# Kernel tuning notes

Measured on AMD Instinct MI355X. Metric: run time of the kernel, lower is better.

The kernel has to match this reference:

```python
import jax, jax.numpy as jnp
import numpy as np

B, S, D, H = 2, 2048, 1024, 16
DK = D // H


def setup_inputs() -> dict:
    key = jax.random.key(0)
    ks = jax.random.split(key, 11)
    s = 1.0 / np.sqrt(D)
    inp = {
        "q": jax.random.normal(ks[0], (B, S, D), jnp.float32),
        "k": jax.random.normal(ks[1], (B, S, D), jnp.float32),
        "v": jax.random.normal(ks[2], (B, S, D), jnp.float32),
        # causal (lower-triangular) decoder mask, broadcast over batch & heads
        "mask": jnp.tril(jnp.ones((S, S), jnp.int32))[None, None, :, :],
        "Wq": jax.random.normal(ks[3], (D, D), jnp.float32) * s,
        "bq": jax.random.normal(ks[4], (D,), jnp.float32) * s,
        "Wk": jax.random.normal(ks[5], (D, D), jnp.float32) * s,
        "bk": jax.random.normal(ks[6], (D,), jnp.float32) * s,
        "Wv": jax.random.normal(ks[7], (D, D), jnp.float32) * s,
        "bv": jax.random.normal(ks[8], (D,), jnp.float32) * s,
        "Wo": jax.random.normal(ks[9], (D, D), jnp.float32) * s,
        "bo": jax.random.normal(ks[10], (D,), jnp.float32) * s,
    }
    return inp


def reference(q, k, v, mask, Wq, bq, Wk, bk, Wv, bv, Wo, bo):
    # projections (nn.Linear: x @ W.T + b)
    def proj(x, W, b):
        return (x @ W.T + b).reshape(B, S, H, DK).transpose(0, 2, 1, 3)  # [B,H,S,DK]

    Q = proj(q, Wq, bq)
    K = proj(k, Wk, bk)
    V = proj(v, Wv, bv)

    scores = jnp.einsum("bhsd,bhtd->bhst", Q, K) / jnp.sqrt(jnp.float32(DK))
    scores = jnp.where(mask == 0, jnp.float32(-1e9), scores)
    attn = jax.nn.softmax(scores, axis=-1)  # dropout=0.0 -> identity
    ctx = jnp.einsum("bhst,bhtd->bhsd", attn, V)
    ctx = ctx.transpose(0, 2, 1, 3).reshape(B, S, D)
    return ctx @ Wo.T + bo
```

## Files before the change

kernel.cpp:

```cpp
#include <hip/hip_runtime.h>

typedef __bf16 bf16;
typedef __bf16 bf16x8 __attribute__((ext_vector_type(8)));
typedef float floatx4 __attribute__((ext_vector_type(4)));

#define NB 2
#define NS 2048
#define ND 1024
#define NH 16
#define NDK 64
#define NM (NB * NS)

__device__ __forceinline__ void async_cp16(const void* g, void* l) {
  __builtin_amdgcn_global_load_lds(
      (const __attribute__((address_space(1))) void*)g,
      (__attribute__((address_space(3))) void*)l, 16, 0, 0);
}

__device__ __forceinline__ bf16x8 cvt8(const float* p) {
  float4 lo = *(const float4*)p, hi = *(const float4*)(p + 4);
  bf16x8 o;
  o[0] = (bf16)lo.x; o[1] = (bf16)lo.y; o[2] = (bf16)lo.z; o[3] = (bf16)lo.w;
  o[4] = (bf16)hi.x; o[5] = (bf16)hi.y; o[6] = (bf16)hi.z; o[7] = (bf16)hi.w;
  return o;
}

struct CvtArgs {
  const float* src[8];
  bf16* dst[8];
  int nblk[8];
  int nseg;
};

__global__ __launch_bounds__(256) void cvt_kernel(CvtArgs a) {
  int b = blockIdx.x, seg = 0;
  while (seg < a.nseg - 1 && b >= a.nblk[seg]) { b -= a.nblk[seg]; ++seg; }
  const size_t idx = ((size_t)b * 256 + threadIdx.x) * 8;
  *(bf16x8*)(a.dst[seg] + idx) = cvt8(a.src[seg] + idx);
}

template <int TM, typename TA, typename TC>
__global__ __launch_bounds__(256) void gemm_dma(
    const TA* __restrict__ A0, const TA* __restrict__ A1, const TA* __restrict__ A2,
    const bf16* __restrict__ W0, const bf16* __restrict__ W1, const bf16* __restrict__ W2,
    const float* __restrict__ bias0, const float* __restrict__ bias1, const float* __restrict__ bias2,
    TC* __restrict__ C0, TC* __restrict__ C1, TC* __restrict__ C2)
{
  const int z = blockIdx.z;
  const TA* A = (z == 0) ? A0 : (z == 1) ? A1 : A2;
  const bf16* W = (z == 0) ? W0 : (z == 1) ? W1 : W2;
  const float* bias = (z == 0) ? bias0 : (z == 1) ? bias1 : bias2;
  TC* C = (z == 0) ? C0 : (z == 1) ? C1 : C2;

  __shared__ bf16 At[TM * 32];
  __shared__ bf16 Bt[128 * 32];

  const int tid = threadIdx.x;
  const int wave = tid >> 6, lane = tid & 63;
  const int q4 = lane >> 4, l15 = lane & 15;
  const int m0 = blockIdx.y * TM, n0 = blockIdx.x * 128;
  constexpr int WM = TM / 2;
  constexpr int MI = WM / 16;
  const int wm = (wave >> 1) * WM, wn = (wave & 1) * 64;

  floatx4 acc[MI][4] = {};

  const bf16* Wg = W + (size_t)(n0 + (lane >> 2)) * ND + (lane & 3) * 8;
  const bf16* Ag = nullptr;
  const float* Af = nullptr;
  const int srow = tid >> 2, sk = (tid & 3) * 8;
  if constexpr (sizeof(TA) == 2)
    Ag = (const bf16*)A + (size_t)(m0 + (lane >> 2)) * ND + (lane & 3) * 8;
  else
    Af = (const float*)A + (size_t)(m0 + srow) * ND + sk;

  for (int k0 = 0; k0 < ND; k0 += 32) {
    bf16x8 a0, a1;
    if constexpr (sizeof(TA) == 4) {
      a0 = cvt8(Af + k0);
      if constexpr (TM == 128) a1 = cvt8(Af + (size_t)64 * ND + k0);
    }
    __syncthreads();
#pragma unroll
    for (int c2 = 0; c2 < 2; ++c2) {
      const int c = wave * 2 + c2;
      async_cp16(Wg + (size_t)c * 16 * ND + k0, &Bt[c * 16 * 32]);
    }
    if constexpr (sizeof(TA) == 2) {
#pragma unroll
      for (int c2 = 0; c2 < TM / 64; ++c2) {
        const int c = wave * (TM / 64) + c2;
        async_cp16(Ag + (size_t)c * 16 * ND + k0, &At[c * 16 * 32]);
      }
    } else {
      *(bf16x8*)&At[srow * 32 + sk] = a0;
      if constexpr (TM == 128) *(bf16x8*)&At[(srow + 64) * 32 + sk] = a1;
    }
    __syncthreads();

    bf16x8 af[MI], bfr[4];
#pragma unroll
    for (int i = 0; i < MI; ++i)
      af[i] = *(const bf16x8*)&At[(wm + i * 16 + l15) * 32 + q4 * 8];
#pragma unroll
    for (int j = 0; j < 4; ++j)
      bfr[j] = *(const bf16x8*)&Bt[(wn + j * 16 + l15) * 32 + q4 * 8];
#pragma unroll
    for (int i = 0; i < MI; ++i)
#pragma unroll
      for (int j = 0; j < 4; ++j)
        acc[i][j] = __builtin_amdgcn_mfma_f32_16x16x32_bf16(af[i], bfr[j], acc[i][j], 0, 0, 0);
  }

#pragma unroll
  for (int j = 0; j < 4; ++j) {
    const int col = n0 + wn + j * 16 + l15;
    const float bv = bias[col];
#pragma unroll
    for (int i = 0; i < MI; ++i) {
      const int rowb = m0 + wm + i * 16 + q4 * 4;
#pragma unroll
      for (int r = 0; r < 4; ++r)
        C[(size_t)(rowb + r) * ND + col] = (TC)(acc[i][j][r] + bv);
    }
  }
}

#define NEGBIG (-1e30f)
#define LDV 72

__global__ __launch_bounds__(256) void attn_kernel(
    const bf16* __restrict__ Q, const bf16* __restrict__ K,
    const bf16* __restrict__ V, bf16* __restrict__ O)
{
  __shared__ bf16 vt[2][64 * LDV];
  __shared__ bf16 pbuf[4][16 * LDV];

  const int bx = blockIdx.x;
  const int h = blockIdx.y, b = blockIdx.z;
  const int tid = threadIdx.x, wave = tid >> 6, lane = tid & 63;
  const int q4 = lane >> 4, l15 = lane & 15;
  const int sl = lane;
  const int dbase = wave * 8;

  const bf16* kp = K + ((size_t)(b * NS) + l15) * ND + h * NDK + q4 * 8;
  const bf16* vp = V + ((size_t)(b * NS) + sl) * ND + h * NDK + dbase;

  bf16x8 qf[2];
  floatx4 oacc[4];
  float psum[4];
  bf16x8 kA[8], vA[2], kB[8], vB[2];

  auto ldK = [&](int j, bf16x8 (&kk)[8]) {
    const bf16* p = kp + (size_t)j * (64 * ND);
#pragma unroll
    for (int nf = 0; nf < 4; ++nf)
#pragma unroll
      for (int t = 0; t < 2; ++t)
        kk[nf * 2 + t] = *(const bf16x8*)(p + (size_t)nf * 16 * ND + t * 32);
  };
  auto ldV = [&](int j, bf16x8 (&vv)[2]) {
    const bf16* p = vp + (size_t)j * (64 * ND);
    vv[0] = *(const bf16x8*)(p);
    vv[1] = *(const bf16x8*)(p + 32);
  };

  auto body = [&](int j, int iq, bf16x8 (&kc)[8], bf16x8 (&vc)[2],
                  bf16x8 (&kn)[8], bf16x8 (&vn)[2]) {
    const int cur = j & 1;
#pragma unroll
    for (int it = 0; it < 2; ++it)
#pragma unroll
      for (int e = 0; e < 8; ++e)
        vt[cur][(dbase + it * 32 + e) * LDV + sl] = vc[it][e];

    floatx4 sf[4];
#pragma unroll
    for (int nf = 0; nf < 4; ++nf) {
      floatx4 s = {0.f, 0.f, 0.f, 0.f};
      s = __builtin_amdgcn_mfma_f32_16x16x32_bf16(qf[0], kc[nf * 2 + 0], s, 0, 0, 0);
      s = __builtin_amdgcn_mfma_f32_16x16x32_bf16(qf[1], kc[nf * 2 + 1], s, 0, 0, 0);
      sf[nf] = s;
    }

    if (j < iq) { ldK(j + 1, kn); ldV(j + 1, vn); }

    __syncthreads();

    if (j == iq) {
#pragma unroll
      for (int nf = 0; nf < 4; ++nf) {
        const int kc2 = nf * 16 + l15;
#pragma unroll
        for (int r = 0; r < 4; ++r)
          if (kc2 > wave * 16 + q4 * 4 + r) sf[nf][r] = NEGBIG;
      }
    }

#pragma unroll
    for (int nf = 0; nf < 4; ++nf)
#pragma unroll
      for (int r = 0; r < 4; ++r) {
        const float pv = exp2f(sf[nf][r]);
        psum[r] += pv;
        pbuf[wave][(q4 * 4 + r) * LDV + nf * 16 + l15] = (bf16)pv;
      }
    __asm__ __volatile__("s_waitcnt lgkmcnt(0)" ::: "memory");

#pragma unroll
    for (int nf = 0; nf < 4; ++nf)
#pragma unroll
      for (int t = 0; t < 2; ++t) {
        bf16x8 pa = *(const bf16x8*)&pbuf[wave][l15 * LDV + t * 32 + q4 * 8];
        bf16x8 vb = *(const bf16x8*)&vt[cur][(nf * 16 + l15) * LDV + t * 32 + q4 * 8];
        oacc[nf] = __builtin_amdgcn_mfma_f32_16x16x32_bf16(pa, vb, oacc[nf], 0, 0, 0);
      }
  };

  for (int ph = 0; ph < 2; ++ph) {
    const int iq = ph ? (31 - bx) : bx;
    __syncthreads();

    const size_t qrow0 = (size_t)(b * NS + iq * 64 + wave * 16 + l15);
#pragma unroll
    for (int t = 0; t < 2; ++t) {
      bf16x8 tmp = *(const bf16x8*)(Q + qrow0 * ND + h * NDK + t * 32 + q4 * 8);
#pragma unroll
      for (int e = 0; e < 8; ++e) qf[t][e] = (bf16)((float)tmp[e] * 0.180336880f);
    }

#pragma unroll
    for (int nf = 0; nf < 4; ++nf) oacc[nf] = floatx4{0.f, 0.f, 0.f, 0.f};
#pragma unroll
    for (int r = 0; r < 4; ++r) psum[r] = 0.f;

    ldK(0, kA); ldV(0, vA);
    for (int j = 0; j <= iq; ++j) {
      if ((j & 1) == 0) body(j, iq, kA, vA, kB, vB);
      else              body(j, iq, kB, vB, kA, vA);
    }

#pragma unroll
    for (int r = 0; r < 4; ++r)
#pragma unroll
      for (int off = 1; off < 16; off <<= 1) psum[r] += __shfl_xor(psum[r], off, 16);

#pragma unroll
    for (int nf = 0; nf < 4; ++nf)
#pragma unroll
      for (int r = 0; r < 4; ++r) {
        const int qrow = iq * 64 + wave * 16 + q4 * 4 + r;
        O[(size_t)(b * NS + qrow) * ND + h * NDK + nf * 16 + l15] =
            (bf16)(oacc[nf][r] / psum[r]);
      }
  }
}

extern "C" void kernel_launch(void* const* d_in, const int* in_sizes, int n_in,
                              void* d_out, int out_size, void* d_ws, size_t ws_size,
                              hipStream_t stream) {
  const float* q  = (const float*)d_in[0];
  const float* k  = (const float*)d_in[1];
  const float* v  = (const float*)d_in[2];
  const float* Wq = (const float*)d_in[4];
  const float* bq = (const float*)d_in[5];
  const float* Wk = (const float*)d_in[6];
  const float* bk = (const float*)d_in[7];
  const float* Wv = (const float*)d_in[8];
  const float* bv = (const float*)d_in[9];
  const float* Wo = (const float*)d_in[10];
  const float* bo = (const float*)d_in[11];
  float* out = (float*)d_out;
  char* w = (char*)d_ws;

  const dim3 attn_grid(NS / 128, NH, NB);

  if (ws_size >= (size_t)56 << 20) {
    bf16* xq = (bf16*)(w);
    bf16* xk = (bf16*)(w + ((size_t)8 << 20));
    bf16* xv = (bf16*)(w + ((size_t)16 << 20));
    bf16* wq = (bf16*)(w + ((size_t)24 << 20));
    bf16* wk = (bf16*)(w + ((size_t)26 << 20));
    bf16* wv = (bf16*)(w + ((size_t)28 << 20));
    bf16* wo = (bf16*)(w + ((size_t)30 << 20));
    bf16* Qb = (bf16*)(w + ((size_t)32 << 20));
    bf16* Kb = (bf16*)(w + ((size_t)40 << 20));
    bf16* Vb = (bf16*)(w + ((size_t)48 << 20));
    bf16* Ob = xq;

    CvtArgs ca{};
    const int b4 = (int)((size_t)NM * ND / 2048);
    const int b1 = (int)((size_t)ND * ND / 2048);
    ca.src[0] = q;  ca.dst[0] = xq; ca.nblk[0] = b4;
    ca.src[1] = k;  ca.dst[1] = xk; ca.nblk[1] = b4;
    ca.src[2] = v;  ca.dst[2] = xv; ca.nblk[2] = b4;
    ca.src[3] = Wq; ca.dst[3] = wq; ca.nblk[3] = b1;
    ca.src[4] = Wk; ca.dst[4] = wk; ca.nblk[4] = b1;
    ca.src[5] = Wv; ca.dst[5] = wv; ca.nblk[5] = b1;
    ca.src[6] = Wo; ca.dst[6] = wo; ca.nblk[6] = b1;
    ca.nseg = 7;
    cvt_kernel<<<3 * b4 + 4 * b1, 256, 0, stream>>>(ca);

    gemm_dma<128, bf16, bf16><<<dim3(8, 32, 3), 256, 0, stream>>>(
        xq, xk, xv, wq, wk, wv, bq, bk, bv, Qb, Kb, Vb);
    attn_kernel<<<attn_grid, 256, 0, stream>>>(Qb, Kb, Vb, Ob);
    gemm_dma<64, bf16, float><<<dim3(8, 64, 1), 256, 0, stream>>>(
        Ob, Ob, Ob, wo, wo, wo, bo, bo, bo, out, out, out);
  } else if (ws_size >= (size_t)40 << 20) {
    bf16* wq = (bf16*)(w);
    bf16* wk = (bf16*)(w + ((size_t)2 << 20));
    bf16* wv = (bf16*)(w + ((size_t)4 << 20));
    bf16* wo = (bf16*)(w + ((size_t)6 << 20));
    bf16* Qb = (bf16*)(w + ((size_t)8 << 20));
    bf16* Kb = (bf16*)(w + ((size_t)16 << 20));
    bf16* Vb = (bf16*)(w + ((size_t)24 << 20));
    bf16* Ob = (bf16*)(w + ((size_t)32 << 20));

    CvtArgs ca{};
    const int b1 = (int)((size_t)ND * ND / 2048);
    ca.src[0] = Wq; ca.dst[0] = wq; ca.nblk[0] = b1;
    ca.src[1] = Wk; ca.dst[1] = wk; ca.nblk[1] = b1;
    ca.src[2] = Wv; ca.dst[2] = wv; ca.nblk[2] = b1;
    ca.src[3] = Wo; ca.dst[3] = wo; ca.nblk[3] = b1;
    ca.nseg = 4;
    cvt_kernel<<<4 * b1, 256, 0, stream>>>(ca);

    gemm_dma<128, float, bf16><<<dim3(8, 32, 3), 256, 0, stream>>>(
        q, k, v, wq, wk, wv, bq, bk, bv, Qb, Kb, Vb);
    attn_kernel<<<attn_grid, 256, 0, stream>>>(Qb, Kb, Vb, Ob);
    gemm_dma<64, bf16, float><<<dim3(8, 64, 1), 256, 0, stream>>>(
        Ob, Ob, Ob, wo, wo, wo, bo, bo, bo, out, out, out);
  }
}
```

Before: 270.5 us.

## Split causal attention KV range across two blocks and combine partial sums

Splits each query tile's key range into two halves handled by separate blocks, doubling the attention grid, then adds a combine kernel that sums the partial outputs and divides by the summed softmax denominators. This raises parallelism across the GPU's compute units for the attention stage. The cost is an extra kernel launch, extra global traffic for the partial outputs and row sums, and rounding the partial outputs to bf16 before they are combined. The method relies on the existing no-max exp2 softmax, so the two partial results can be added directly.

```diff
diff --git a/kernel.cpp b/kernel.cpp
--- a/kernel.cpp
+++ b/kernel.cpp
@@ -126,8 +126,172 @@
   }
 }
 
-#define NEGBIG (-1e30f)
 #define LDV 72
+
+__global__ __launch_bounds__(256) void attn_split(
+    const bf16* __restrict__ Q, const bf16* __restrict__ K,
+    const bf16* __restrict__ V, bf16* __restrict__ Oh0,
+    bf16* __restrict__ Oh1, float* __restrict__ Ps)
+{
+  __shared__ bf16 vt[2][64 * LDV];
+  __shared__ bf16 pbuf[4][16 * LDV];
+
+  const int bx = blockIdx.x;
+  const int h = blockIdx.y;
+  const int b = blockIdx.z & 1, half = blockIdx.z >> 1;
+  bf16* Oh = half ? Oh1 : Oh0;
+  const int tid = threadIdx.x, wave = tid >> 6, lane = tid & 63;
+  const int q4 = lane >> 4, l15 = lane & 15;
+  const int sl = lane;
+  const int dbase = wave * 8;
+
+  const bf16* kp = K + ((size_t)(b * NS) + l15) * ND + h * NDK + q4 * 8;
+  const bf16* vp = V + ((size_t)(b * NS) + sl) * ND + h * NDK + dbase;
+
+  bf16x8 qf[2];
+  floatx4 oacc[4];
+  float psum[4];
+  bf16x8 kA[8], vA[2], kB[8], vB[2];
+
+  auto ldK = [&](int j, bf16x8 (&kk)[8]) {
+    const bf16* p = kp + (size_t)j * (64 * ND);
+#pragma unroll
+    for (int nf = 0; nf < 4; ++nf)
+#pragma unroll
+      for (int t = 0; t < 2; ++t)
+        kk[nf * 2 + t] = *(const bf16x8*)(p + (size_t)nf * 16 * ND + t * 32);
+  };
+  auto ldV = [&](int j, bf16x8 (&vv)[2]) {
+    const bf16* p = vp + (size_t)j * (64 * ND);
+    vv[0] = *(const bf16x8*)(p);
+    vv[1] = *(const bf16x8*)(p + 32);
+  };
+
+  auto body = [&](int j, int iq, int je, bf16x8 (&kc)[8], bf16x8 (&vc)[2],
+                  bf16x8 (&kn)[8], bf16x8 (&vn)[2]) {
+    const int cur = j & 1;
+#pragma unroll
+    for (int it = 0; it < 2; ++it)
+#pragma unroll
+      for (int e = 0; e < 8; ++e)
+        vt[cur][(dbase + it * 32 + e) * LDV + sl] = vc[it][e];
+
+    floatx4 sf[4];
+#pragma unroll
+    for (int nf = 0; nf < 4; ++nf) {
+      floatx4 s = {0.f, 0.f, 0.f, 0.f};
+      s = __builtin_amdgcn_mfma_f32_16x16x32_bf16(qf[0], kc[nf * 2 + 0], s, 0, 0, 0);
+      s = __builtin_amdgcn_mfma_f32_16x16x32_bf16(qf[1], kc[nf * 2 + 1], s, 0, 0, 0);
+      sf[nf] = s;
+    }
+
+    if (j + 1 < je) { ldK(j + 1, kn); ldV(j + 1, vn); }
+
+    __syncthreads();
+
+    if (j == iq) {
+#pragma unroll
+      for (int nf = 0; nf < 4; ++nf) {
+        const int kc2 = nf * 16 + l15;
+#pragma unroll
+        for (int r = 0; r < 4; ++r)
+          if (kc2 > wave * 16 + q4 * 4 + r) sf[nf][r] = -1e30f;
+      }
+    }
+
+#pragma unroll
+    for (int nf = 0; nf < 4; ++nf)
+#pragma unroll
+      for (int r = 0; r < 4; ++r) {
+        const float pv = exp2f(sf[nf][r]);
+        psum[r] += pv;
+        pbuf[wave][(q4 * 4 + r) * LDV + nf * 16 + l15] = (bf16)pv;
+      }
+    __asm__ __volatile__("s_waitcnt lgkmcnt(0)" ::: "memory");
+
+#pragma unroll
+    for (int nf = 0; nf < 4; ++nf)
+#pragma unroll
+      for (int t = 0; t < 2; ++t) {
+        bf16x8 pa = *(const bf16x8*)&pbuf[wave][l15 * LDV + t * 32 + q4 * 8];
+        bf16x8 vb = *(const bf16x8*)&vt[cur][(nf * 16 + l15) * LDV + t * 32 + q4 * 8];
+        oacc[nf] = __builtin_amdgcn_mfma_f32_16x16x32_bf16(pa, vb, oacc[nf], 0, 0, 0);
+      }
+  };
+
+  for (int ph = 0; ph < 2; ++ph) {
+    const int iq = ph ? (31 - bx) : bx;
+    const int n = iq + 1;
+    const int h0 = (n + 1) >> 1;
+    const int js = half ? h0 : 0;
+    const int je = half ? n : h0;
+    __syncthreads();
+
+    const size_t qrow0 = (size_t)(b * NS + iq * 64 + wave * 16 + l15);
+#pragma unroll
+    for (int t = 0; t < 2; ++t) {
+      bf16x8 tmp = *(const bf16x8*)(Q + qrow0 * ND + h * NDK + t * 32 + q4 * 8);
+#pragma unroll
+      for (int e = 0; e < 8; ++e) qf[t][e] = (bf16)((float)tmp[e] * 0.180336880f);
+    }
+
+#pragma unroll
+    for (int nf = 0; nf < 4; ++nf) oacc[nf] = floatx4{0.f, 0.f, 0.f, 0.f};
+#pragma unroll
+    for (int r = 0; r < 4; ++r) psum[r] = 0.f;
+
+    if (je > js) {
+      ldK(js, kA); ldV(js, vA);
+      const int cnt = je - js;
+      for (int jj = 0; jj < cnt; ++jj) {
+        const int j = js + jj;
+        if ((jj & 1) == 0) body(j, iq, je, kA, vA, kB, vB);
+        else               body(j, iq, je, kB, vB, kA, vA);
+      }
+    }
+
+#pragma unroll
+    for (int r = 0; r < 4; ++r)
+#pragma unroll
+      for (int off = 1; off < 16; off <<= 1) psum[r] += __shfl_xor(psum[r], off, 16);
+
+#pragma unroll
+    for (int nf = 0; nf < 4; ++nf)
+#pragma unroll
+      for (int r = 0; r < 4; ++r) {
+        const int qrow = iq * 64 + wave * 16 + q4 * 4 + r;
+        Oh[(size_t)(b * NS + qrow) * ND + h * NDK + nf * 16 + l15] = (bf16)oacc[nf][r];
+      }
+    if (l15 == 0) {
+#pragma unroll
+      for (int r = 0; r < 4; ++r) {
+        const int qrow = iq * 64 + wave * 16 + q4 * 4 + r;
+        Ps[(((size_t)half * NB + b) * NH + h) * NS + qrow] = psum[r];
+      }
+    }
+  }
+}
+
+__global__ __launch_bounds__(256) void attn_combine(
+    const bf16* __restrict__ Oh0, const bf16* __restrict__ Oh1,
+    const float* __restrict__ Ps, bf16* __restrict__ Ob)
+{
+  const size_t g = (size_t)blockIdx.x * 256 + threadIdx.x;
+  const int row = (int)(g >> 7);
+  const int col = ((int)g & 127) * 8;
+  const int b = row >> 11, srow = row & (NS - 1);
+  const int h = col >> 6;
+  const float p0 = Ps[(((size_t)0 * NB + b) * NH + h) * NS + srow];
+  const float p1 = Ps[(((size_t)1 * NB + b) * NH + h) * NS + srow];
+  const float inv = 1.0f / (p0 + p1);
+  const size_t off = (size_t)row * ND + col;
+  bf16x8 o0 = *(const bf16x8*)(Oh0 + off);
+  bf16x8 o1 = *(const bf16x8*)(Oh1 + off);
+  bf16x8 o;
+#pragma unroll
+  for (int e = 0; e < 8; ++e) o[e] = (bf16)(((float)o0[e] + (float)o1[e]) * inv);
+  *(bf16x8*)(Ob + off) = o;
+}
 
 __global__ __launch_bounds__(256) void attn_kernel(
     const bf16* __restrict__ Q, const bf16* __restrict__ K,
@@ -184,7 +348,6 @@
     }
 
     if (j < iq) { ldK(j + 1, kn); ldV(j + 1, vn); }
-
     __syncthreads();
 
     if (j == iq) {
@@ -193,7 +356,7 @@
         const int kc2 = nf * 16 + l15;
 #pragma unroll
         for (int r = 0; r < 4; ++r)
-          if (kc2 > wave * 16 + q4 * 4 + r) sf[nf][r] = NEGBIG;
+          if (kc2 > wave * 16 + q4 * 4 + r) sf[nf][r] = -1e30f;
       }
     }
 
@@ -273,8 +436,6 @@
   float* out = (float*)d_out;
   char* w = (char*)d_ws;
 
-  const dim3 attn_grid(NS / 128, NH, NB);
-
   if (ws_size >= (size_t)56 << 20) {
     bf16* xq = (bf16*)(w);
     bf16* xk = (bf16*)(w + ((size_t)8 << 20));
@@ -286,6 +447,9 @@
     bf16* Qb = (bf16*)(w + ((size_t)32 << 20));
     bf16* Kb = (bf16*)(w + ((size_t)40 << 20));
     bf16* Vb = (bf16*)(w + ((size_t)48 << 20));
+    bf16* Oh0 = xk;
+    bf16* Oh1 = xv;
+    float* Ps = (float*)wq;
     bf16* Ob = xq;
 
     CvtArgs ca{};
@@ -303,7 +467,8 @@
 
     gemm_dma<128, bf16, bf16><<<dim3(8, 32, 3), 256, 0, stream>>>(
         xq, xk, xv, wq, wk, wv, bq, bk, bv, Qb, Kb, Vb);
-    attn_kernel<<<attn_grid, 256, 0, stream>>>(Qb, Kb, Vb, Ob);
+    attn_split<<<dim3(16, NH, NB * 2), 256, 0, stream>>>(Qb, Kb, Vb, Oh0, Oh1, Ps);
+    attn_combine<<<(int)((size_t)NM * ND / 8 / 256), 256, 0, stream>>>(Oh0, Oh1, Ps, Ob);
     gemm_dma<64, bf16, float><<<dim3(8, 64, 1), 256, 0, stream>>>(
         Ob, Ob, Ob, wo, wo, wo, bo, bo, bo, out, out, out);
   } else if (ws_size >= (size_t)40 << 20) {
@@ -327,7 +492,7 @@
 
     gemm_dma<128, float, bf16><<<dim3(8, 32, 3), 256, 0, stream>>>(
         q, k, v, wq, wk, wv, bq, bk, bv, Qb, Kb, Vb);
-    attn_kernel<<<attn_grid, 256, 0, stream>>>(Qb, Kb, Vb, Ob);
+    attn_kernel<<<dim3(16, NH, NB), 256, 0, stream>>>(Qb, Kb, Vb, Ob);
     gemm_dma<64, bf16, float><<<dim3(8, 64, 1), 256, 0, stream>>>(
         Ob, Ob, Ob, wo, wo, wo, bo, bo, bo, out, out, out);
   }
```

Result: slower. 276.5 us (+2.2%).
